# Kernel optimization log

Measured on AMD Instinct MI355X. Metric: run time of the kernel, lower is better.

## Reference

```python
import jax, jax.numpy as jnp
import numpy as np

D_MODEL = 1024
NUM_HEADS = 16
D_K = D_MODEL // NUM_HEADS


def setup_inputs() -> dict:
    key = jax.random.key(0)
    ks = jax.random.split(key, 9)
    s = 1.0 / np.sqrt(D_MODEL)
    inp = {
        "x": jax.random.normal(ks[0], (2, 2048, D_MODEL), dtype=jnp.float32),
        "Wq": jax.random.uniform(ks[1], (D_MODEL, D_MODEL), jnp.float32, -s, s),
        "bq": jax.random.uniform(ks[2], (D_MODEL,), jnp.float32, -s, s),
        "Wk": jax.random.uniform(ks[3], (D_MODEL, D_MODEL), jnp.float32, -s, s),
        "bk": jax.random.uniform(ks[4], (D_MODEL,), jnp.float32, -s, s),
        "Wv": jax.random.uniform(ks[5], (D_MODEL, D_MODEL), jnp.float32, -s, s),
        "bv": jax.random.uniform(ks[6], (D_MODEL,), jnp.float32, -s, s),
        "Wo": jax.random.uniform(ks[7], (D_MODEL, D_MODEL), jnp.float32, -s, s),
        "bo": jax.random.uniform(ks[8], (D_MODEL,), jnp.float32, -s, s),
    }
    return inp


def reference(x, Wq, bq, Wk, bk, Wv, bv, Wo, bo):
    B, S, _ = x.shape
    # projections (torch Linear: y = x @ W.T + b)
    q = x @ Wq.T + bq
    k = x @ Wk.T + bk
    v = x @ Wv.T + bv
    # [B, H, S, Dk]
    q = q.reshape(B, S, NUM_HEADS, D_K).transpose(0, 2, 1, 3)
    k = k.reshape(B, S, NUM_HEADS, D_K).transpose(0, 2, 1, 3)
    v = v.reshape(B, S, NUM_HEADS, D_K).transpose(0, 2, 1, 3)
    scale = 1.0 / np.sqrt(D_K).astype(np.float32)
    energy = jnp.einsum("bhqd,bhkd->bhqk", q, k) * scale
    attn = jax.nn.softmax(energy, axis=-1)
    out = jnp.einsum("bhqk,bhkd->bhqd", attn, v)
    out = out.transpose(0, 2, 1, 3).reshape(B, S, D_MODEL)
    return out @ Wo.T + bo
```

## Files before the change

kernel.cpp:

```cpp
#include <hip/hip_runtime.h>
#include <hip/hip_bf16.h>
#include <cstdint>

typedef __bf16 bf16;
typedef __bf16 bf16x4 __attribute__((ext_vector_type(4)));
typedef __bf16 bf16x8 __attribute__((ext_vector_type(8)));
typedef float f32x4 __attribute__((ext_vector_type(4)));

#define DM   1024
#define SEQ  2048
#define NH   16
#define DKH  64

__device__ __forceinline__ bf16x8 ld8(const bf16* p) {
    return *reinterpret_cast<const bf16x8*>(p);
}

__device__ __forceinline__ void gld16(const void* g, void* lds) {
    __builtin_amdgcn_global_load_lds(
        (__attribute__((address_space(1))) void*)(uintptr_t)g,
        (__attribute__((address_space(3))) void*)(uint32_t)(uintptr_t)lds,
        16, 0, 0);
}

__device__ __forceinline__ f32x4 mfma16(bf16x8 a, bf16x8 b, f32x4 c) {
    return __builtin_amdgcn_mfma_f32_16x16x32_bf16(a, b, c, 0, 0, 0);
}

__global__ __launch_bounds__(256) void cvt_all(
    const float4* __restrict__ x,  const float4* __restrict__ wq,
    const float4* __restrict__ wk, const float4* __restrict__ wv,
    const float4* __restrict__ wo,
    ushort4* __restrict__ xb,  ushort4* __restrict__ wqb,
    ushort4* __restrict__ wkb, ushort4* __restrict__ wvb,
    ushort4* __restrict__ wob) {
    int i = blockIdx.x * 256 + threadIdx.x;
    const float4* src;
    ushort4* dst;
    int off;
    if (i < 1048576) {
        src = x; dst = xb; off = i;
    } else {
        int r = i - 1048576;
        int sel = r >> 18;
        off = r & 262143;
        src = sel == 0 ? wq : sel == 1 ? wk : sel == 2 ? wv : wo;
        dst = sel == 0 ? wqb : sel == 1 ? wkb : sel == 2 ? wvb : wob;
    }
    float4 f = src[off];
    ushort4 u;
    u.x = __builtin_bit_cast(unsigned short, (bf16)f.x);
    u.y = __builtin_bit_cast(unsigned short, (bf16)f.y);
    u.z = __builtin_bit_cast(unsigned short, (bf16)f.z);
    u.w = __builtin_bit_cast(unsigned short, (bf16)f.w);
    dst[off] = u;
}

template <int OUT_MODE>
__device__ __forceinline__ void gemm_body(const bf16* __restrict__ A,
                                          const bf16* __restrict__ W,
                                          const float* __restrict__ bias,
                                          void* __restrict__ outp,
                                          int m0, int n0, float scale,
                                          bf16* __restrict__ As,
                                          bf16* __restrict__ Bs) {
    constexpr int K = DM, BK = 64;

    const int t     = threadIdx.x;
    const int lane  = t & 63;
    const int row16 = lane & 15, grp = lane >> 4;
    const int wave  = t >> 6;
    const int wr    = (wave >> 1) * 64;
    const int wc    = (wave & 1) * 64;

    f32x4 acc[4][4] = {};

    const int sc = (t & 7) * 8;
    const bf16* Ag = A + (size_t)(m0 + (t >> 3)) * K + sc;
    const bf16* Wg = W + (size_t)(n0 + (t >> 3)) * K + sc;
    bf16* Asw = &As[t * 8];
    bf16* Bsw = &Bs[t * 8];

    for (int kt = 0; kt < K; kt += BK) {
        __syncthreads();
#pragma unroll
        for (int i = 0; i < 4; ++i) {
            gld16(Ag + (size_t)i * 32 * K + kt, Asw + i * 2048);
            gld16(Wg + (size_t)i * 32 * K + kt, Bsw + i * 2048);
        }
        __syncthreads();
#pragma unroll
        for (int kk = 0; kk < BK; kk += 32) {
            bf16x8 af[4], bfr[4];
#pragma unroll
            for (int m = 0; m < 4; ++m)
                af[m] = ld8(&As[(wr + m * 16 + row16) * BK + kk + grp * 8]);
#pragma unroll
            for (int n = 0; n < 4; ++n)
                bfr[n] = ld8(&Bs[(wc + n * 16 + row16) * BK + kk + grp * 8]);
#pragma unroll
            for (int m = 0; m < 4; ++m)
#pragma unroll
                for (int n = 0; n < 4; ++n)
                    acc[m][n] = mfma16(af[m], bfr[n], acc[m][n]);
        }
    }

    if constexpr (OUT_MODE == 2) {
        __syncthreads();
        bf16* Tw = (wave < 2) ? As + wave * 4096 : Bs + (wave - 2) * 4096;
        const int b = m0 >> 11;
        const int tokbase = (m0 & 2047) + wr;
#pragma unroll
        for (int n = 0; n < 4; ++n) {
            const int dim = n * 16 + row16;
            const float bv = bias[n0 + wc + dim];
#pragma unroll
            for (int m = 0; m < 4; ++m) {
                bf16x4 w4 = {(bf16)(acc[m][n][0] + bv), (bf16)(acc[m][n][1] + bv),
                             (bf16)(acc[m][n][2] + bv), (bf16)(acc[m][n][3] + bv)};
                const int slot = (m * 2 + (grp >> 1)) ^ (dim & 7);
                *reinterpret_cast<bf16x4*>(&Tw[dim * 64 + slot * 8 + (grp & 1) * 4]) = w4;
            }
        }
        asm volatile("" ::: "memory");
#pragma unroll
        for (int r = 0; r < 8; ++r) {
            const int dim = (lane >> 3) + 8 * r;
            const int ts  = lane & 7;
            bf16x8 v = ld8(&Tw[dim * 64 + ((ts ^ (dim & 7)) * 8)]);
            const int col = n0 + wc + dim;
            bf16* dst = (bf16*)outp +
                ((size_t)(b * NH + (col >> 6)) * DKH + (col & 63)) * SEQ +
                tokbase + ts * 8;
            *reinterpret_cast<bf16x8*>(dst) = v;
        }
    } else {
#pragma unroll
        for (int n = 0; n < 4; ++n) {
            const int col = n0 + wc + n * 16 + row16;
            const float bv = bias[col];
#pragma unroll
            for (int m = 0; m < 4; ++m) {
                const int row = m0 + wr + m * 16 + grp * 4;
#pragma unroll
                for (int j = 0; j < 4; ++j) {
                    float v = (acc[m][n][j] + bv) * scale;
                    if constexpr (OUT_MODE == 1)
                        ((float*)outp)[(size_t)(row + j) * DM + col] = v;
                    else
                        ((bf16*)outp)[(size_t)(row + j) * DM + col] = (bf16)v;
                }
            }
        }
    }
}

__global__ __launch_bounds__(256, 4) void gemm_qkv(
    const bf16* __restrict__ xb,
    const bf16* __restrict__ wqb, const bf16* __restrict__ wkb, const bf16* __restrict__ wvb,
    const float* __restrict__ bq, const float* __restrict__ bk, const float* __restrict__ bv,
    bf16* __restrict__ q, bf16* __restrict__ k, bf16* __restrict__ vt) {
    __shared__ __attribute__((aligned(16))) bf16 As[128 * 64];
    __shared__ __attribute__((aligned(16))) bf16 Bs[128 * 64];
    const int sel = blockIdx.y >> 3;
    const int m0 = blockIdx.x * 128, n0 = (blockIdx.y & 7) * 128;
    if (sel == 0) {
        gemm_body<0>(xb, wqb, bq, q, m0, n0, 0.18033688f, As, Bs);
    } else if (sel == 1) {
        gemm_body<0>(xb, wkb, bk, k, m0, n0, 1.0f, As, Bs);
    } else {
        gemm_body<2>(xb, wvb, bv, vt, m0, n0, 1.0f, As, Bs);
    }
}

__global__ __launch_bounds__(256, 4) void gemm_out(
    const bf16* __restrict__ ab, const bf16* __restrict__ wob,
    const float* __restrict__ bo, float* __restrict__ out) {
    __shared__ __attribute__((aligned(16))) bf16 As[128 * 64];
    __shared__ __attribute__((aligned(16))) bf16 Bs[128 * 64];
    gemm_body<1>(ab, wob, bo, out, blockIdx.x * 128, blockIdx.y * 128, 1.0f, As, Bs);
}

__global__ __launch_bounds__(256) void attn(const bf16* __restrict__ Q,
                                            const bf16* __restrict__ K,
                                            const bf16* __restrict__ VT,
                                            bf16* __restrict__ O) {
    __shared__ __attribute__((aligned(16))) bf16 Ks[2][64 * 64];
    __shared__ __attribute__((aligned(16))) bf16 Vs[2][64 * 64];
    __shared__ __attribute__((aligned(16))) bf16 Ps[4][32 * 64];

    const int t = threadIdx.x, lane = t & 63, wave = t >> 6;
    const int r16 = lane & 15, g = lane >> 4;

    int id = blockIdx.x;
    id = (id & 7) * 64 + (id >> 3);
    const int qt = id & 15, h = (id >> 4) & 15, b = id >> 8;

    const bf16* Qb = Q + ((size_t)b * SEQ + qt * 128) * DM + h * DKH;
    const bf16* Kb = K + (size_t)b * SEQ * DM + h * DKH;
    const bf16* Vb = VT + (size_t)((b * NH + h) * DKH) * SEQ;

    bf16x8 qf[2][2];
#pragma unroll
    for (int u = 0; u < 2; ++u)
#pragma unroll
        for (int p = 0; p < 2; ++p)
            qf[u][p] = ld8(Qb + (size_t)(wave * 32 + u * 16 + r16) * DM + p * 32 + g * 8);

    const bf16 one = (bf16)1.0f;
    const bf16x8 ones8 = {one, one, one, one, one, one, one, one};

    f32x4 o[2][4] = {};
    f32x4 ol[2] = {};

    const int sr = t >> 3, scs = t & 7;

    auto STAGE = [&](int bsel, int kt) {
#pragma unroll
        for (int i = 0; i < 2; ++i) {
            const int r = i * 32 + sr;
            const int cs = (scs ^ (r & 7)) * 8;
            gld16(Kb + (size_t)(kt + r) * DM + cs, &Ks[bsel][i * 2048 + t * 8]);
            gld16(Vb + (size_t)r * SEQ + kt + cs, &Vs[bsel][i * 2048 + t * 8]);
        }
    };

    STAGE(0, 0);
    __syncthreads();

    int cur = 0;
    for (int kt = 0; kt < SEQ; kt += 64) {
        if (kt + 64 < SEQ) STAGE(cur ^ 1, kt + 64);
        const bf16* KsB = Ks[cur];
        const bf16* VsB = Vs[cur];

        f32x4 s[2][4];
        __builtin_amdgcn_s_setprio(1);
#pragma unroll
        for (int n = 0; n < 4; ++n) {
            const int row = n * 16 + r16;
            const bf16x8 kf0 = ld8(&KsB[row * 64 + ((g) ^ (row & 7)) * 8]);
            const bf16x8 kf1 = ld8(&KsB[row * 64 + ((4 + g) ^ (row & 7)) * 8]);
#pragma unroll
            for (int u = 0; u < 2; ++u) {
                f32x4 a = {};
                a = mfma16(kf0, qf[u][0], a);
                a = mfma16(kf1, qf[u][1], a);
                s[u][n] = a;
            }
        }
        __builtin_amdgcn_s_setprio(0);

        bf16x8 vtf[4][2];
#pragma unroll
        for (int n = 0; n < 4; ++n) {
            const int row = n * 16 + r16;
#pragma unroll
            for (int p = 0; p < 2; ++p)
                vtf[n][p] = ld8(&VsB[row * 64 + ((p * 4 + g) ^ (row & 7)) * 8]);
        }

        bf16* Pw = Ps[wave];
        const int sw = r16 & 7;
#pragma unroll
        for (int u = 0; u < 2; ++u) {
            const int rb = (u * 16 + r16) * 64;
#pragma unroll
            for (int n = 0; n < 4; ++n) {
                f32x4 pv;
#pragma unroll
                for (int j = 0; j < 4; ++j)
                    pv[j] = __builtin_amdgcn_exp2f(s[u][n][j]);
                bf16x4 w4 = {(bf16)pv[0], (bf16)pv[1], (bf16)pv[2], (bf16)pv[3]};
                const int slot = (n * 2 + (g >> 1)) ^ sw;
                *reinterpret_cast<bf16x4*>(&Pw[rb + slot * 8 + (g & 1) * 4]) = w4;
            }
        }
        asm volatile("" ::: "memory");

        __builtin_amdgcn_s_setprio(1);
#pragma unroll
        for (int u = 0; u < 2; ++u) {
            const int rb = (u * 16 + r16) * 64;
            const bf16x8 pa0 = ld8(&Pw[rb + ((g ^ sw) * 8)]);
            const bf16x8 pa1 = ld8(&Pw[rb + (((4 + g) ^ sw) * 8)]);
#pragma unroll
            for (int n = 0; n < 4; ++n) {
                o[u][n] = mfma16(pa0, vtf[n][0], o[u][n]);
                o[u][n] = mfma16(pa1, vtf[n][1], o[u][n]);
            }
            ol[u] = mfma16(pa0, ones8, ol[u]);
            ol[u] = mfma16(pa1, ones8, ol[u]);
        }
        __builtin_amdgcn_s_setprio(0);

        __syncthreads();
        cur ^= 1;
    }

#pragma unroll
    for (int u = 0; u < 2; ++u) {
#pragma unroll
        for (int j = 0; j < 4; ++j) {
            const float inv = 1.0f / ol[u][j];
            bf16* orow = O + ((size_t)b * SEQ + qt * 128 + wave * 32 + u * 16 + g * 4 + j) * DM
                         + h * DKH + r16;
#pragma unroll
            for (int n = 0; n < 4; ++n)
                orow[n * 16] = (bf16)(o[u][n][j] * inv);
        }
    }
}

extern "C" void kernel_launch(void* const* d_in, const int* in_sizes, int n_in,
                              void* d_out, int out_size, void* d_ws, size_t ws_size,
                              hipStream_t stream) {
    const float* x  = (const float*)d_in[0];
    const float* Wq = (const float*)d_in[1];
    const float* bq = (const float*)d_in[2];
    const float* Wk = (const float*)d_in[3];
    const float* bk = (const float*)d_in[4];
    const float* Wv = (const float*)d_in[5];
    const float* bv = (const float*)d_in[6];
    const float* Wo = (const float*)d_in[7];
    const float* bo = (const float*)d_in[8];
    float* out = (float*)d_out;

    char* ws = (char*)d_ws;
    bf16* xb  = (bf16*)(ws + 0);
    bf16* wqb = (bf16*)(ws + 8388608);
    bf16* wkb = (bf16*)(ws + 10485760);
    bf16* wvb = (bf16*)(ws + 12582912);
    bf16* wob = (bf16*)(ws + 14680064);
    bf16* qb  = (bf16*)(ws + 16777216);
    bf16* kb  = (bf16*)(ws + 25165824);
    bf16* ab  = (bf16*)(ws + 33554432);
    bf16* vtb = (bf16*)(ws + 41943040);

    cvt_all<<<8192, 256, 0, stream>>>(
        (const float4*)x, (const float4*)Wq, (const float4*)Wk,
        (const float4*)Wv, (const float4*)Wo,
        (ushort4*)xb, (ushort4*)wqb, (ushort4*)wkb, (ushort4*)wvb, (ushort4*)wob);

    gemm_qkv<<<dim3(32, 24), 256, 0, stream>>>(xb, wqb, wkb, wvb, bq, bk, bv, qb, kb, vtb);

    attn<<<dim3(512), 256, 0, stream>>>(qb, kb, vtb, ab);

    gemm_out<<<dim3(32, 8), 256, 0, stream>>>(ab, wob, bo, out);
}
```

Baseline: 122.3 us.

## Switch attention to 32x32x16 MFMA with register-resident P via permlane swap

Rewrites the attention inner loop to use 32x32x16 bf16 MFMA tiles instead of 16x16x32. The exponentiated scores are packed to bf16 and rearranged between lanes with v_permlane32_swap, so P feeds the PV MFMA directly from registers and the per-wave LDS staging buffer and its round trip go away. The row sum is now accumulated with scalar adds plus a cross-half shuffle instead of extra MFMAs against a ones vector. The cost is more complex lane-layout reasoning and a scattered per-element output store pattern.

```diff
diff --git a/kernel.cpp b/kernel.cpp
--- a/kernel.cpp
+++ b/kernel.cpp
@@ -6,6 +6,8 @@
 typedef __bf16 bf16x4 __attribute__((ext_vector_type(4)));
 typedef __bf16 bf16x8 __attribute__((ext_vector_type(8)));
 typedef float f32x4 __attribute__((ext_vector_type(4)));
+typedef float f32x16 __attribute__((ext_vector_type(16)));
+typedef unsigned int u32x4 __attribute__((ext_vector_type(4)));
 
 #define DM   1024
 #define SEQ  2048
@@ -25,6 +27,18 @@
 
 __device__ __forceinline__ f32x4 mfma16(bf16x8 a, bf16x8 b, f32x4 c) {
     return __builtin_amdgcn_mfma_f32_16x16x32_bf16(a, b, c, 0, 0, 0);
+}
+__device__ __forceinline__ f32x16 mfma32(bf16x8 a, bf16x8 b, f32x16 c) {
+    return __builtin_amdgcn_mfma_f32_32x32x16_bf16(a, b, c, 0, 0, 0);
+}
+
+__device__ __forceinline__ unsigned pkbf(float lo, float hi) {
+    unsigned r;
+    asm("v_cvt_pk_bf16_f32 %0, %1, %2" : "=v"(r) : "v"(lo), "v"(hi));
+    return r;
+}
+__device__ __forceinline__ void plswap(unsigned& a, unsigned& b) {
+    asm volatile("v_permlane32_swap_b32 %0, %1" : "+v"(a), "+v"(b));
 }
 
 __global__ __launch_bounds__(256) void cvt_all(
@@ -188,10 +202,9 @@
                                             bf16* __restrict__ O) {
     __shared__ __attribute__((aligned(16))) bf16 Ks[2][64 * 64];
     __shared__ __attribute__((aligned(16))) bf16 Vs[2][64 * 64];
-    __shared__ __attribute__((aligned(16))) bf16 Ps[4][32 * 64];
 
     const int t = threadIdx.x, lane = t & 63, wave = t >> 6;
-    const int r16 = lane & 15, g = lane >> 4;
+    const int l31 = lane & 31, hi = lane >> 5;
 
     int id = blockIdx.x;
     id = (id & 7) * 64 + (id >> 3);
@@ -201,18 +214,13 @@
     const bf16* Kb = K + (size_t)b * SEQ * DM + h * DKH;
     const bf16* Vb = VT + (size_t)((b * NH + h) * DKH) * SEQ;
 
-    bf16x8 qf[2][2];
-#pragma unroll
-    for (int u = 0; u < 2; ++u)
-#pragma unroll
-        for (int p = 0; p < 2; ++p)
-            qf[u][p] = ld8(Qb + (size_t)(wave * 32 + u * 16 + r16) * DM + p * 32 + g * 8);
-
-    const bf16 one = (bf16)1.0f;
-    const bf16x8 ones8 = {one, one, one, one, one, one, one, one};
-
-    f32x4 o[2][4] = {};
-    f32x4 ol[2] = {};
+    bf16x8 qf[4];
+#pragma unroll
+    for (int c = 0; c < 4; ++c)
+        qf[c] = ld8(Qb + (size_t)(wave * 32 + l31) * DM + c * 16 + hi * 8);
+
+    f32x16 o[2] = {};
+    float L = 0.f;
 
     const int sr = t >> 3, scs = t & 7;
 
@@ -235,63 +243,45 @@
         const bf16* KsB = Ks[cur];
         const bf16* VsB = Vs[cur];
 
-        f32x4 s[2][4];
+        u32x4 up[4];
+#pragma unroll
+        for (int sub = 0; sub < 2; ++sub) {
+            const int krow = sub * 32 + l31;
+            const int ksw  = krow & 7;
+            f32x16 ss = {};
+            __builtin_amdgcn_s_setprio(1);
+#pragma unroll
+            for (int c = 0; c < 4; ++c) {
+                const bf16x8 kf = ld8(&KsB[krow * 64 + (((c * 2 + hi) ^ ksw) * 8)]);
+                ss = mfma32(kf, qf[c], ss);
+            }
+            __builtin_amdgcn_s_setprio(0);
+            float e[16];
+#pragma unroll
+            for (int r = 0; r < 16; ++r) {
+                e[r] = __builtin_amdgcn_exp2f(ss[r]);
+                L += e[r];
+            }
+            unsigned u0 = pkbf(e[0],  e[1]),  u1 = pkbf(e[2],  e[3]);
+            unsigned u2 = pkbf(e[4],  e[5]),  u3 = pkbf(e[6],  e[7]);
+            unsigned u4 = pkbf(e[8],  e[9]),  u5 = pkbf(e[10], e[11]);
+            unsigned u6 = pkbf(e[12], e[13]), u7 = pkbf(e[14], e[15]);
+            plswap(u0, u2); plswap(u1, u3);
+            plswap(u4, u6); plswap(u5, u7);
+            up[sub * 2]     = u32x4{u0, u1, u2, u3};
+            up[sub * 2 + 1] = u32x4{u4, u5, u6, u7};
+        }
+
         __builtin_amdgcn_s_setprio(1);
 #pragma unroll
-        for (int n = 0; n < 4; ++n) {
-            const int row = n * 16 + r16;
-            const bf16x8 kf0 = ld8(&KsB[row * 64 + ((g) ^ (row & 7)) * 8]);
-            const bf16x8 kf1 = ld8(&KsB[row * 64 + ((4 + g) ^ (row & 7)) * 8]);
-#pragma unroll
-            for (int u = 0; u < 2; ++u) {
-                f32x4 a = {};
-                a = mfma16(kf0, qf[u][0], a);
-                a = mfma16(kf1, qf[u][1], a);
-                s[u][n] = a;
-            }
-        }
-        __builtin_amdgcn_s_setprio(0);
-
-        bf16x8 vtf[4][2];
-#pragma unroll
-        for (int n = 0; n < 4; ++n) {
-            const int row = n * 16 + r16;
-#pragma unroll
-            for (int p = 0; p < 2; ++p)
-                vtf[n][p] = ld8(&VsB[row * 64 + ((p * 4 + g) ^ (row & 7)) * 8]);
-        }
-
-        bf16* Pw = Ps[wave];
-        const int sw = r16 & 7;
-#pragma unroll
-        for (int u = 0; u < 2; ++u) {
-            const int rb = (u * 16 + r16) * 64;
-#pragma unroll
-            for (int n = 0; n < 4; ++n) {
-                f32x4 pv;
-#pragma unroll
-                for (int j = 0; j < 4; ++j)
-                    pv[j] = __builtin_amdgcn_exp2f(s[u][n][j]);
-                bf16x4 w4 = {(bf16)pv[0], (bf16)pv[1], (bf16)pv[2], (bf16)pv[3]};
-                const int slot = (n * 2 + (g >> 1)) ^ sw;
-                *reinterpret_cast<bf16x4*>(&Pw[rb + slot * 8 + (g & 1) * 4]) = w4;
-            }
-        }
-        asm volatile("" ::: "memory");
-
-        __builtin_amdgcn_s_setprio(1);
-#pragma unroll
-        for (int u = 0; u < 2; ++u) {
-            const int rb = (u * 16 + r16) * 64;
-            const bf16x8 pa0 = ld8(&Pw[rb + ((g ^ sw) * 8)]);
-            const bf16x8 pa1 = ld8(&Pw[rb + (((4 + g) ^ sw) * 8)]);
-#pragma unroll
-            for (int n = 0; n < 4; ++n) {
-                o[u][n] = mfma16(pa0, vtf[n][0], o[u][n]);
-                o[u][n] = mfma16(pa1, vtf[n][1], o[u][n]);
-            }
-            ol[u] = mfma16(pa0, ones8, ol[u]);
-            ol[u] = mfma16(pa1, ones8, ol[u]);
+        for (int dt = 0; dt < 2; ++dt) {
+            const int vrow = dt * 32 + l31;
+            const int vsw  = vrow & 7;
+#pragma unroll
+            for (int kc = 0; kc < 4; ++kc) {
+                const bf16x8 vf = ld8(&VsB[vrow * 64 + (((kc * 2 + hi) ^ vsw) * 8)]);
+                o[dt] = mfma32(__builtin_bit_cast(bf16x8, up[kc]), vf, o[dt]);
+            }
         }
         __builtin_amdgcn_s_setprio(0);
 
@@ -299,18 +289,20 @@
         cur ^= 1;
     }
 
-#pragma unroll
-    for (int u = 0; u < 2; ++u) {
-#pragma unroll
-        for (int j = 0; j < 4; ++j) {
-            const float inv = 1.0f / ol[u][j];
-            bf16* orow = O + ((size_t)b * SEQ + qt * 128 + wave * 32 + u * 16 + g * 4 + j) * DM
-                         + h * DKH + r16;
-#pragma unroll
-            for (int n = 0; n < 4; ++n)
-                orow[n * 16] = (bf16)(o[u][n][j] * inv);
-        }
-    }
+    const float Lfull = L + __shfl_xor(L, 32);
+    const float inv = 1.0f / Lfull;
+    float invr[16];
+#pragma unroll
+    for (int r = 0; r < 16; ++r)
+        invr[r] = __shfl(inv, (r & 3) + 8 * (r >> 2) + 4 * hi);
+#pragma unroll
+    for (int dt = 0; dt < 2; ++dt)
+#pragma unroll
+        for (int r = 0; r < 16; ++r) {
+            const int ql = (r & 3) + 8 * (r >> 2) + 4 * hi;
+            O[((size_t)b * SEQ + qt * 128 + wave * 32 + ql) * DM
+              + h * DKH + dt * 32 + l31] = (bf16)(o[dt][r] * invr[r]);
+        }
 }
 
 extern "C" void kernel_launch(void* const* d_in, const int* in_sizes, int n_in,
```

Result: no change. 122.8 us (+0.4%).
